# Optimization experiments

Measured on AMD Instinct MI355X. Metric: run time of the kernel, lower is better.

Reference implementation:

```python
import jax, jax.numpy as jnp
import numpy as np

D_MODEL = 512
N_HEADS = 8
D_K = D_MODEL // N_HEADS


def setup_inputs() -> dict:
    key = jax.random.key(0)
    kq, kk, kv = jax.random.split(key, 3)
    shape = (4, 2048, D_MODEL)
    return {
        "Q": jax.random.normal(kq, shape, dtype=jnp.float32),
        "K": jax.random.normal(kk, shape, dtype=jnp.float32),
        "V": jax.random.normal(kv, shape, dtype=jnp.float32),
    }


def reference(Q, K, V):
    B, S, _ = Q.shape
    # [B, S, H, Dk] -> [B, H, S, Dk]
    q = Q.reshape(B, S, N_HEADS, D_K).transpose(0, 2, 1, 3)
    k = K.reshape(B, S, N_HEADS, D_K).transpose(0, 2, 1, 3)
    v = V.reshape(B, S, N_HEADS, D_K).transpose(0, 2, 1, 3)
    scale = 1.0 / (D_K ** 0.5)
    # [B, H, S, S] scores (faithful to original: full matrix materialized)
    scores = jnp.einsum("bhqd,bhkd->bhqk", q, k) * scale
    attn = jax.nn.softmax(scores, axis=-1)
    out = jnp.einsum("bhqk,bhkd->bhqd", attn, v)
    # [B, H, S, Dk] -> [B, S, D_MODEL]
    return out.transpose(0, 2, 1, 3).reshape(B, S, D_MODEL)
```

## Files before the change

### kernel.cpp

```cpp
#include <hip/hip_runtime.h>
#include <hip/hip_bf16.h>

#define SEQ    2048
#define DMODEL 512
#define NH     8
#define QBLK   128
#define KVB    64

#if __has_builtin(__builtin_amdgcn_exp2f)
#define EXPFN(x) __builtin_amdgcn_exp2f(x)
#define QSCALE 0.18033688011112042f
#else
#define EXPFN(x) __expf(x)
#define QSCALE 0.125f
#endif
#define THR 8.0f

typedef __attribute__((ext_vector_type(8)))  short bf16x8;
typedef __attribute__((ext_vector_type(16))) float f32x16;
typedef __attribute__((ext_vector_type(2)))  int   i32x2;

#define MFMA32(A, B, C) __builtin_amdgcn_mfma_f32_32x32x16_bf16(A, B, C, 0, 0, 0)

__device__ __forceinline__ unsigned short f2bf(float f) {
  union { float f; unsigned u; } x; x.f = f;
  return (unsigned short)((x.u + 0x7FFFu + ((x.u >> 16) & 1u)) >> 16);
}

__device__ __forceinline__ int cvtpk(float lo, float hi) {
  int r;
  asm("v_cvt_pk_bf16_f32 %0, %1, %2" : "=v"(r) : "v"(lo), "v"(hi));
  return r;
}

__device__ __forceinline__ i32x2 plswap(int a, int b) {
#if __has_builtin(__builtin_amdgcn_permlane32_swap)
  return __builtin_amdgcn_permlane32_swap(a, b, false, false);
#else
  int a2 = __shfl_xor(a, 32), b2 = __shfl_xor(b, 32);
  int hi = (threadIdx.x >> 5) & 1;
  i32x2 r; r.x = hi ? b2 : a; r.y = hi ? b : a2; return r;
#endif
}

__device__ __forceinline__ void gload16(const void* g, void* l) {
  __builtin_amdgcn_global_load_lds(
      (const __attribute__((address_space(1))) void*)g,
      (__attribute__((address_space(3))) void*)l, 16, 0, 0);
}


__global__ void prep_kv(const float* __restrict__ K, const float* __restrict__ V,
                        unsigned short* __restrict__ kb, unsigned short* __restrict__ vb) {
  if (blockIdx.x < 2048) {
    int gid = blockIdx.x * 256 + threadIdx.x;
    int g  = gid & 7;
    int s  = (gid >> 3) & (SEQ - 1);
    int bh = gid >> 14;
    int b = bh >> 3, h = bh & 7;
    const float* src = K + ((size_t)(b * SEQ + s) * DMODEL) + h * 64 + (g << 3);
    float4 a = ((const float4*)src)[0];
    float4 c = ((const float4*)src)[1];
    bf16x8 w;
    w[0] = (short)f2bf(a.x); w[1] = (short)f2bf(a.y);
    w[2] = (short)f2bf(a.z); w[3] = (short)f2bf(a.w);
    w[4] = (short)f2bf(c.x); w[5] = (short)f2bf(c.y);
    w[6] = (short)f2bf(c.z); w[7] = (short)f2bf(c.w);
    int r = s & 63;
    int slot = ((((r >> 5) << 3) + g) ^ (r & 15));
    unsigned short* dst = kb + ((size_t)bh * SEQ + (s & ~63)) * 64
                             + ((r & 31) << 7) + (slot << 3);
    *(bf16x8*)dst = w;
  } else {
    int bt = blockIdx.x - 2048;
    int bh = bt >> 5, tile = bt & 31;
    int b = bh >> 3, h = bh & 7;
    int t  = threadIdx.x;
    int d  = t & 63;
    int kg = t >> 6;
    const float* src = V + ((size_t)(b * SEQ + tile * 64 + kg * 16) * DMODEL) + h * 64 + d;
    float v[16];
#pragma unroll
    for (int j = 0; j < 16; ++j) v[j] = src[(size_t)j * DMODEL];
    bf16x8 lo, hi;
#pragma unroll
    for (int j = 0; j < 8; ++j) { lo[j] = (short)f2bf(v[j]); hi[j] = (short)f2bf(v[8 + j]); }
    unsigned short* base = vb + ((size_t)bt << 12);
    int g0 = kg << 1, g1 = (kg << 1) | 1;
    int rb = (((d >> 5) << 3));
    int s0 = ((rb + g0) ^ (d & 15));
    int s1 = ((rb + g1) ^ (d & 15));
    unsigned short* row = base + ((d & 31) << 7);
    *(bf16x8*)(row + (s0 << 3)) = lo;
    *(bf16x8*)(row + (s1 << 3)) = hi;
  }
}

__global__ __launch_bounds__(256, 2)
void fa_fwd(const float* __restrict__ Q, const unsigned short* __restrict__ Kb,
            const unsigned short* __restrict__ Vb, float* __restrict__ O) {
  __shared__ unsigned short kt[2][KVB * 64];
  __shared__ unsigned short vt[2][64 * KVB];

  const int tid = threadIdx.x;
  const int wv  = tid >> 6;
  const int ln  = tid & 63;
  const int l31 = ln & 31;
  const int hi  = ln >> 5;

  const int orig = blockIdx.x;
  const int wgid = (orig & 7) * 64 + (orig >> 3);
  const int bh = wgid >> 4;
  const int qt = wgid & 15;
  const int b = bh >> 3, h = bh & 7;

  const float* Qh = Q + (size_t)b * SEQ * DMODEL + (size_t)h * 64;
  float*       Oh = O + (size_t)b * SEQ * DMODEL + (size_t)h * 64;
  const unsigned short* Kh = Kb + (size_t)bh * SEQ * 64;
  const unsigned short* Vh = Vb + (size_t)bh * SEQ * 64;

  const int q = qt * QBLK + wv * 32 + l31;

  bf16x8 qf[4];
  {
    const float* qp = Qh + (size_t)q * DMODEL + (hi << 3);
#pragma unroll
    for (int t = 0; t < 4; ++t) {
      float4 a = *(const float4*)(qp + 16 * t);
      float4 c = *(const float4*)(qp + 16 * t + 4);
      bf16x8 w;
      w[0] = (short)f2bf(a.x * QSCALE); w[1] = (short)f2bf(a.y * QSCALE);
      w[2] = (short)f2bf(a.z * QSCALE); w[3] = (short)f2bf(a.w * QSCALE);
      w[4] = (short)f2bf(c.x * QSCALE); w[5] = (short)f2bf(c.y * QSCALE);
      w[6] = (short)f2bf(c.z * QSCALE); w[7] = (short)f2bf(c.w * QSCALE);
      qf[t] = w;
    }
  }

  const int rowb = l31 << 7;
  int ca[4], cb[4];
#pragma unroll
  for (int t = 0; t < 4; ++t) {
    int g = 2 * t + hi;
    ca[t] = rowb + (((g)     ^ (l31 & 15)) << 3);
    cb[t] = rowb + (((8 + g) ^ (l31 & 15)) << 3);
  }

  f32x16 o0 = {}, o1 = {};
  float m = -__builtin_inff();
  float l = 0.f;

#define STAGE(T, B)                                                        \
  do {                                                                     \
    const char* gk = (const char*)(Kh + (size_t)(T) * KVB * 64);           \
    const char* gv = (const char*)(Vh + (size_t)(T) * KVB * 64);           \
    char* lk = (char*)&kt[(B)][0];                                         \
    char* lv = (char*)&vt[(B)][0];                                         \
    gload16(gk + (((wv)     * 64 + ln) << 4), lk + ((wv)     << 10));      \
    gload16(gk + (((wv + 4) * 64 + ln) << 4), lk + ((wv + 4) << 10));      \
    gload16(gv + (((wv)     * 64 + ln) << 4), lv + ((wv)     << 10));      \
    gload16(gv + (((wv + 4) * 64 + ln) << 4), lv + ((wv + 4) << 10));      \
  } while (0)

  auto tile_compute = [&](const unsigned short* ktb, const unsigned short* vtb) {
    f32x16 s0 = {}, s1 = {};
#pragma unroll
    for (int ks = 0; ks < 4; ++ks) {
      bf16x8 k0 = *(const bf16x8*)&ktb[ca[ks]];
      bf16x8 k1 = *(const bf16x8*)&ktb[cb[ks]];
      __builtin_amdgcn_s_setprio(1);
      s0 = MFMA32(k0, qf[ks], s0);
      s1 = MFMA32(k1, qf[ks], s1);
      __builtin_amdgcn_s_setprio(0);
    }

    float pm = fmaxf(s0[0], s0[1]);
#pragma unroll
    for (int j = 2; j < 16; ++j) pm = fmaxf(pm, s0[j]);
#pragma unroll
    for (int j = 0; j < 16; ++j) pm = fmaxf(pm, s1[j]);
    pm = fmaxf(pm, __shfl_xor(pm, 32));

    if (__any(pm > m + THR)) {
      float mn   = fmaxf(m, pm);
      float corr = EXPFN(m - mn);
      m = mn;
      l *= corr;
#pragma unroll
      for (int j = 0; j < 16; ++j) { o0[j] *= corr; o1[j] *= corr; }
    }

#pragma unroll
    for (int ks = 0; ks < 4; ++ks) {
      float e[8];
#pragma unroll
      for (int j = 0; j < 8; ++j) {
        float sv = (ks < 2) ? s0[(ks & 1) * 8 + j] : s1[(ks & 1) * 8 + j];
        e[j] = EXPFN(sv - m);
      }
      l += ((e[0] + e[1]) + (e[2] + e[3])) + ((e[4] + e[5]) + (e[6] + e[7]));
      i32x2 r0 = plswap(cvtpk(e[0], e[1]), cvtpk(e[4], e[5]));
      i32x2 r1 = plswap(cvtpk(e[2], e[3]), cvtpk(e[6], e[7]));
      union { int i[4]; bf16x8 v; } pa;
      pa.i[0] = r0.x; pa.i[1] = r1.x; pa.i[2] = r0.y; pa.i[3] = r1.y;

      bf16x8 v0 = *(const bf16x8*)&vtb[ca[ks]];
      bf16x8 v1 = *(const bf16x8*)&vtb[cb[ks]];
      __builtin_amdgcn_s_setprio(1);
      o0 = MFMA32(v0, pa.v, o0);
      o1 = MFMA32(v1, pa.v, o1);
      __builtin_amdgcn_s_setprio(0);
    }
  };

  STAGE(0, 0);
  __syncthreads();

  for (int t = 0; t < SEQ / KVB; t += 2) {
    STAGE(t + 1, 1);
    tile_compute(kt[0], vt[0]);
    __syncthreads();
    if (t + 2 < SEQ / KVB) STAGE(t + 2, 0);
    tile_compute(kt[1], vt[1]);
    __syncthreads();
  }

  l += __shfl_xor(l, 32);
  float rinv = 1.0f / l;
  float* op = Oh + (size_t)q * DMODEL;
#pragma unroll
  for (int r4 = 0; r4 < 4; ++r4) {
    float4 w0, w1;
    w0.x = o0[4 * r4 + 0] * rinv; w0.y = o0[4 * r4 + 1] * rinv;
    w0.z = o0[4 * r4 + 2] * rinv; w0.w = o0[4 * r4 + 3] * rinv;
    w1.x = o1[4 * r4 + 0] * rinv; w1.y = o1[4 * r4 + 1] * rinv;
    w1.z = o1[4 * r4 + 2] * rinv; w1.w = o1[4 * r4 + 3] * rinv;
    *(float4*)(op + 8 * r4 + 4 * hi)      = w0;
    *(float4*)(op + 32 + 8 * r4 + 4 * hi) = w1;
  }
}

extern "C" void kernel_launch(void* const* d_in, const int* in_sizes, int n_in,
                              void* d_out, int out_size, void* d_ws, size_t ws_size,
                              hipStream_t stream) {
  const float* Q = (const float*)d_in[0];
  const float* K = (const float*)d_in[1];
  const float* V = (const float*)d_in[2];
  float* O = (float*)d_out;
  unsigned short* kb = (unsigned short*)d_ws;
  unsigned short* vb = kb + (size_t)32 * SEQ * 64;
  prep_kv<<<3072, 256, 0, stream>>>(K, V, kb, vb);
  fa_fwd<<<512, 256, 0, stream>>>(Q, kb, vb, O);
}
```

Before: 63.12 us.

## Software-pipeline QK of next tile with softmax/PV of current tile

Splits the per-tile compute into a QK stage and a softmax+PV stage, and issues the QK MFMAs for tile t+1 before the softmax and PV of tile t so matrix work overlaps with exp/reduction work. LDS staging grows from double to quadruple buffering, with loads issued two tiles ahead. This doubles shared memory use and keeps two score accumulator sets live, which raises register pressure and could hurt occupancy at two blocks per CU.

```diff
diff --git a/kernel.cpp b/kernel.cpp
--- a/kernel.cpp
+++ b/kernel.cpp
@@ -6,6 +6,7 @@
 #define NH     8
 #define QBLK   128
 #define KVB    64
+#define NT     (SEQ / KVB)
 
 #if __has_builtin(__builtin_amdgcn_exp2f)
 #define EXPFN(x) __builtin_amdgcn_exp2f(x)
@@ -99,8 +100,8 @@
 __global__ __launch_bounds__(256, 2)
 void fa_fwd(const float* __restrict__ Q, const unsigned short* __restrict__ Kb,
             const unsigned short* __restrict__ Vb, float* __restrict__ O) {
-  __shared__ unsigned short kt[2][KVB * 64];
-  __shared__ unsigned short vt[2][64 * KVB];
+  __shared__ unsigned short kt[4][KVB * 64];
+  __shared__ unsigned short vt[4][64 * KVB];
 
   const int tid = threadIdx.x;
   const int wv  = tid >> 6;
@@ -147,6 +148,7 @@
   }
 
   f32x16 o0 = {}, o1 = {};
+  f32x16 sA0, sA1, sB0, sB1;
   float m = -__builtin_inff();
   float l = 0.f;
 
@@ -162,18 +164,21 @@
     gload16(gv + (((wv + 4) * 64 + ln) << 4), lv + ((wv + 4) << 10));      \
   } while (0)
 
-  auto tile_compute = [&](const unsigned short* ktb, const unsigned short* vtb) {
-    f32x16 s0 = {}, s1 = {};
+  auto qk = [&](const unsigned short* ktb, f32x16& t0, f32x16& t1) {
+    f32x16 u0 = {}, u1 = {};
 #pragma unroll
     for (int ks = 0; ks < 4; ++ks) {
       bf16x8 k0 = *(const bf16x8*)&ktb[ca[ks]];
       bf16x8 k1 = *(const bf16x8*)&ktb[cb[ks]];
       __builtin_amdgcn_s_setprio(1);
-      s0 = MFMA32(k0, qf[ks], s0);
-      s1 = MFMA32(k1, qf[ks], s1);
+      u0 = MFMA32(k0, qf[ks], u0);
+      u1 = MFMA32(k1, qf[ks], u1);
       __builtin_amdgcn_s_setprio(0);
     }
-
+    t0 = u0; t1 = u1;
+  };
+
+  auto smpv = [&](f32x16& s0, f32x16& s1, const unsigned short* vtb) {
     float pm = fmaxf(s0[0], s0[1]);
 #pragma unroll
     for (int j = 2; j < 16; ++j) pm = fmaxf(pm, s0[j]);
@@ -213,16 +218,24 @@
     }
   };
 
+#define ITER(T, BC, BN, BS, SC0, SC1, SN0, SN1)                            \
+  do {                                                                     \
+    if ((T) + 2 < NT) STAGE((T) + 2, BS);                                  \
+    if ((T) + 1 < NT) qk(kt[BN], SN0, SN1);                                \
+    smpv(SC0, SC1, vt[BC]);                                                \
+    __syncthreads();                                                       \
+  } while (0)
+
   STAGE(0, 0);
+  STAGE(1, 1);
   __syncthreads();
-
-  for (int t = 0; t < SEQ / KVB; t += 2) {
-    STAGE(t + 1, 1);
-    tile_compute(kt[0], vt[0]);
-    __syncthreads();
-    if (t + 2 < SEQ / KVB) STAGE(t + 2, 0);
-    tile_compute(kt[1], vt[1]);
-    __syncthreads();
+  qk(kt[0], sA0, sA1);
+
+  for (int t = 0; t < NT; t += 4) {
+    ITER(t + 0, 0, 1, 2, sA0, sA1, sB0, sB1);
+    ITER(t + 1, 1, 2, 3, sB0, sB1, sA0, sA1);
+    ITER(t + 2, 2, 3, 0, sA0, sA1, sB0, sB1);
+    ITER(t + 3, 3, 0, 1, sB0, sB1, sA0, sA1);
   }
 
   l += __shfl_xor(l, 32);
```

After: 63.30 us. About the same (+0.3%).

## Split KV sequence in two halves with fp16 partials and a combine kernel

Applied to the files above, without the earlier changes.

Adds a split-KV (flash-decoding style) path: each workgroup handles half of the key/value tiles for a query block, writing normalized fp16 partial outputs plus (max, sum) statistics, and a separate combine kernel merges the two halves into the fp32 output. This doubles the grid from 512 to 1024 workgroups with higher occupancy hints, so the GPU's CUs are better filled. The cost is an extra kernel launch, extra workspace traffic for the partials, and fp16 rounding of the partial outputs. The path only runs when the workspace is large enough; otherwise the original kernel is used.

```diff
diff --git a/kernel.cpp b/kernel.cpp
--- a/kernel.cpp
+++ b/kernel.cpp
@@ -1,11 +1,14 @@
 #include <hip/hip_runtime.h>
 #include <hip/hip_bf16.h>
+#include <hip/hip_fp16.h>
 
 #define SEQ    2048
 #define DMODEL 512
 #define NH     8
 #define QBLK   128
 #define KVB    64
+#define NT     (SEQ / KVB)
+#define NT_H   (NT / 2)
 
 #if __has_builtin(__builtin_amdgcn_exp2f)
 #define EXPFN(x) __builtin_amdgcn_exp2f(x)
@@ -16,9 +19,11 @@
 #endif
 #define THR 8.0f
 
-typedef __attribute__((ext_vector_type(8)))  short bf16x8;
-typedef __attribute__((ext_vector_type(16))) float f32x16;
-typedef __attribute__((ext_vector_type(2)))  int   i32x2;
+typedef __attribute__((ext_vector_type(8)))  short     bf16x8;
+typedef __attribute__((ext_vector_type(16))) float     f32x16;
+typedef __attribute__((ext_vector_type(2)))  int       i32x2;
+typedef __attribute__((ext_vector_type(4)))  _Float16  f16x4;
+typedef __attribute__((ext_vector_type(8)))  _Float16  f16x8;
 
 #define MFMA32(A, B, C) __builtin_amdgcn_mfma_f32_32x32x16_bf16(A, B, C, 0, 0, 0)
 
@@ -48,7 +53,6 @@
       (const __attribute__((address_space(1))) void*)g,
       (__attribute__((address_space(3))) void*)l, 16, 0, 0);
 }
-
 
 __global__ void prep_kv(const float* __restrict__ K, const float* __restrict__ V,
                         unsigned short* __restrict__ kb, unsigned short* __restrict__ vb) {
@@ -96,61 +100,7 @@
   }
 }
 
-__global__ __launch_bounds__(256, 2)
-void fa_fwd(const float* __restrict__ Q, const unsigned short* __restrict__ Kb,
-            const unsigned short* __restrict__ Vb, float* __restrict__ O) {
-  __shared__ unsigned short kt[2][KVB * 64];
-  __shared__ unsigned short vt[2][64 * KVB];
-
-  const int tid = threadIdx.x;
-  const int wv  = tid >> 6;
-  const int ln  = tid & 63;
-  const int l31 = ln & 31;
-  const int hi  = ln >> 5;
-
-  const int orig = blockIdx.x;
-  const int wgid = (orig & 7) * 64 + (orig >> 3);
-  const int bh = wgid >> 4;
-  const int qt = wgid & 15;
-  const int b = bh >> 3, h = bh & 7;
-
-  const float* Qh = Q + (size_t)b * SEQ * DMODEL + (size_t)h * 64;
-  float*       Oh = O + (size_t)b * SEQ * DMODEL + (size_t)h * 64;
-  const unsigned short* Kh = Kb + (size_t)bh * SEQ * 64;
-  const unsigned short* Vh = Vb + (size_t)bh * SEQ * 64;
-
-  const int q = qt * QBLK + wv * 32 + l31;
-
-  bf16x8 qf[4];
-  {
-    const float* qp = Qh + (size_t)q * DMODEL + (hi << 3);
-#pragma unroll
-    for (int t = 0; t < 4; ++t) {
-      float4 a = *(const float4*)(qp + 16 * t);
-      float4 c = *(const float4*)(qp + 16 * t + 4);
-      bf16x8 w;
-      w[0] = (short)f2bf(a.x * QSCALE); w[1] = (short)f2bf(a.y * QSCALE);
-      w[2] = (short)f2bf(a.z * QSCALE); w[3] = (short)f2bf(a.w * QSCALE);
-      w[4] = (short)f2bf(c.x * QSCALE); w[5] = (short)f2bf(c.y * QSCALE);
-      w[6] = (short)f2bf(c.z * QSCALE); w[7] = (short)f2bf(c.w * QSCALE);
-      qf[t] = w;
-    }
-  }
-
-  const int rowb = l31 << 7;
-  int ca[4], cb[4];
-#pragma unroll
-  for (int t = 0; t < 4; ++t) {
-    int g = 2 * t + hi;
-    ca[t] = rowb + (((g)     ^ (l31 & 15)) << 3);
-    cb[t] = rowb + (((8 + g) ^ (l31 & 15)) << 3);
-  }
-
-  f32x16 o0 = {}, o1 = {};
-  float m = -__builtin_inff();
-  float l = 0.f;
-
-#define STAGE(T, B)                                                        \
+#define STAGE_BODY(T, B)                                                   \
   do {                                                                     \
     const char* gk = (const char*)(Kh + (size_t)(T) * KVB * 64);           \
     const char* gv = (const char*)(Vh + (size_t)(T) * KVB * 64);           \
@@ -162,6 +112,61 @@
     gload16(gv + (((wv + 4) * 64 + ln) << 4), lv + ((wv + 4) << 10));      \
   } while (0)
 
+__global__ __launch_bounds__(256, 4)
+void fa_fwd_split(const float* __restrict__ Q, const unsigned short* __restrict__ Kb,
+                  const unsigned short* __restrict__ Vb,
+                  _Float16* __restrict__ opart, float2* __restrict__ ml) {
+  __shared__ unsigned short kt[2][KVB * 64];
+  __shared__ unsigned short vt[2][64 * KVB];
+
+  const int tid = threadIdx.x;
+  const int wv  = tid >> 6;
+  const int ln  = tid & 63;
+  const int l31 = ln & 31;
+  const int hi  = ln >> 5;
+
+  const int orig = blockIdx.x;
+  const int wgid = (orig & 7) * 128 + (orig >> 3);
+  const int bh   = wgid >> 5;
+  const int qt   = (wgid >> 1) & 15;
+  const int half = wgid & 1;
+  const int b = bh >> 3, h = bh & 7;
+
+  const float* Qh = Q + (size_t)b * SEQ * DMODEL + (size_t)h * 64;
+  const unsigned short* Kh = Kb + (size_t)bh * SEQ * 64 + (size_t)half * NT_H * KVB * 64;
+  const unsigned short* Vh = Vb + (size_t)bh * SEQ * 64 + (size_t)half * NT_H * KVB * 64;
+
+  const int qrow = qt * QBLK + wv * 32 + l31;
+
+  bf16x8 qf[4];
+  {
+    const float* qp = Qh + (size_t)qrow * DMODEL + (hi << 3);
+#pragma unroll
+    for (int t = 0; t < 4; ++t) {
+      float4 a = *(const float4*)(qp + 16 * t);
+      float4 c = *(const float4*)(qp + 16 * t + 4);
+      bf16x8 w;
+      w[0] = (short)f2bf(a.x * QSCALE); w[1] = (short)f2bf(a.y * QSCALE);
+      w[2] = (short)f2bf(a.z * QSCALE); w[3] = (short)f2bf(a.w * QSCALE);
+      w[4] = (short)f2bf(c.x * QSCALE); w[5] = (short)f2bf(c.y * QSCALE);
+      w[6] = (short)f2bf(c.z * QSCALE); w[7] = (short)f2bf(c.w * QSCALE);
+      qf[t] = w;
+    }
+  }
+
+  const int rowb = l31 << 7;
+  int ca[4], cb[4];
+#pragma unroll
+  for (int t = 0; t < 4; ++t) {
+    int g = 2 * t + hi;
+    ca[t] = rowb + (((g)     ^ (l31 & 15)) << 3);
+    cb[t] = rowb + (((8 + g) ^ (l31 & 15)) << 3);
+  }
+
+  f32x16 o0 = {}, o1 = {};
+  float m = -__builtin_inff();
+  float l = 0.f;
+
   auto tile_compute = [&](const unsigned short* ktb, const unsigned short* vtb) {
     f32x16 s0 = {}, s1 = {};
 #pragma unroll
@@ -213,14 +218,178 @@
     }
   };
 
-  STAGE(0, 0);
+  STAGE_BODY(0, 0);
   __syncthreads();
-
-  for (int t = 0; t < SEQ / KVB; t += 2) {
-    STAGE(t + 1, 1);
+  for (int t = 0; t < NT_H; t += 2) {
+    STAGE_BODY(t + 1, 1);
     tile_compute(kt[0], vt[0]);
     __syncthreads();
-    if (t + 2 < SEQ / KVB) STAGE(t + 2, 0);
+    if (t + 2 < NT_H) STAGE_BODY(t + 2, 0);
+    tile_compute(kt[1], vt[1]);
+    __syncthreads();
+  }
+
+  l += __shfl_xor(l, 32);
+  float rinv = 1.0f / l;
+  const size_t row = (size_t)bh * SEQ + qrow;
+  if (hi == 0) ml[(size_t)half * 32 * SEQ + row] = float2{m, l};
+  _Float16* op = opart + (size_t)half * 32 * SEQ * 64 + row * 64;
+#pragma unroll
+  for (int r4 = 0; r4 < 4; ++r4) {
+    f16x4 w0, w1;
+#pragma unroll
+    for (int j = 0; j < 4; ++j) {
+      w0[j] = (_Float16)(o0[4 * r4 + j] * rinv);
+      w1[j] = (_Float16)(o1[4 * r4 + j] * rinv);
+    }
+    *(f16x4*)(op + 8 * r4 + 4 * hi)      = w0;
+    *(f16x4*)(op + 32 + 8 * r4 + 4 * hi) = w1;
+  }
+}
+
+__global__ __launch_bounds__(256)
+void fa_combine(const _Float16* __restrict__ opart, const float2* __restrict__ ml,
+                float* __restrict__ O) {
+  int idx  = blockIdx.x * 256 + threadIdx.x;
+  int dg   = idx & 7;
+  int qrow = (idx >> 3) & (SEQ - 1);
+  int bh   = idx >> 14;
+  size_t row = (size_t)bh * SEQ + qrow;
+
+  float2 a = ml[row];
+  float2 c = ml[(size_t)32 * SEQ + row];
+  float M  = fmaxf(a.x, c.x);
+  float w1 = a.y * EXPFN(a.x - M);
+  float w2 = c.y * EXPFN(c.x - M);
+  float inv = 1.0f / (w1 + w2);
+  w1 *= inv; w2 *= inv;
+
+  f16x8 h1 = *(const f16x8*)(opart + row * 64 + dg * 8);
+  f16x8 h2 = *(const f16x8*)(opart + (size_t)32 * SEQ * 64 + row * 64 + dg * 8);
+
+  int b = bh >> 3, h = bh & 7;
+  float* out = O + ((size_t)(b * SEQ + qrow)) * DMODEL + h * 64 + dg * 8;
+  float4 v0, v1;
+  v0.x = w1 * (float)h1[0] + w2 * (float)h2[0];
+  v0.y = w1 * (float)h1[1] + w2 * (float)h2[1];
+  v0.z = w1 * (float)h1[2] + w2 * (float)h2[2];
+  v0.w = w1 * (float)h1[3] + w2 * (float)h2[3];
+  v1.x = w1 * (float)h1[4] + w2 * (float)h2[4];
+  v1.y = w1 * (float)h1[5] + w2 * (float)h2[5];
+  v1.z = w1 * (float)h1[6] + w2 * (float)h2[6];
+  v1.w = w1 * (float)h1[7] + w2 * (float)h2[7];
+  ((float4*)out)[0] = v0;
+  ((float4*)out)[1] = v1;
+}
+
+__global__ __launch_bounds__(256, 2)
+void fa_fwd(const float* __restrict__ Q, const unsigned short* __restrict__ Kb,
+            const unsigned short* __restrict__ Vb, float* __restrict__ O) {
+  __shared__ unsigned short kt[2][KVB * 64];
+  __shared__ unsigned short vt[2][64 * KVB];
+
+  const int tid = threadIdx.x;
+  const int wv  = tid >> 6;
+  const int ln  = tid & 63;
+  const int l31 = ln & 31;
+  const int hi  = ln >> 5;
+
+  const int orig = blockIdx.x;
+  const int wgid = (orig & 7) * 64 + (orig >> 3);
+  const int bh = wgid >> 4;
+  const int qt = wgid & 15;
+  const int b = bh >> 3, h = bh & 7;
+
+  const float* Qh = Q + (size_t)b * SEQ * DMODEL + (size_t)h * 64;
+  float*       Oh = O + (size_t)b * SEQ * DMODEL + (size_t)h * 64;
+  const unsigned short* Kh = Kb + (size_t)bh * SEQ * 64;
+  const unsigned short* Vh = Vb + (size_t)bh * SEQ * 64;
+
+  const int q = qt * QBLK + wv * 32 + l31;
+
+  bf16x8 qf[4];
+  {
+    const float* qp = Qh + (size_t)q * DMODEL + (hi << 3);
+#pragma unroll
+    for (int t = 0; t < 4; ++t) {
+      float4 a = *(const float4*)(qp + 16 * t);
+      float4 c = *(const float4*)(qp + 16 * t + 4);
+      bf16x8 w;
+      w[0] = (short)f2bf(a.x * QSCALE); w[1] = (short)f2bf(a.y * QSCALE);
+      w[2] = (short)f2bf(a.z * QSCALE); w[3] = (short)f2bf(a.w * QSCALE);
+      w[4] = (short)f2bf(c.x * QSCALE); w[5] = (short)f2bf(c.y * QSCALE);
+      w[6] = (short)f2bf(c.z * QSCALE); w[7] = (short)f2bf(c.w * QSCALE);
+      qf[t] = w;
+    }
+  }
+
+  const int rowb = l31 << 7;
+  int ca[4], cb[4];
+#pragma unroll
+  for (int t = 0; t < 4; ++t) {
+    int g = 2 * t + hi;
+    ca[t] = rowb + (((g)     ^ (l31 & 15)) << 3);
+    cb[t] = rowb + (((8 + g) ^ (l31 & 15)) << 3);
+  }
+
+  f32x16 o0 = {}, o1 = {};
+  float m = -__builtin_inff();
+  float l = 0.f;
+
+  auto tile_compute = [&](const unsigned short* ktb, const unsigned short* vtb) {
+    f32x16 s0 = {}, s1 = {};
+#pragma unroll
+    for (int ks = 0; ks < 4; ++ks) {
+      bf16x8 k0 = *(const bf16x8*)&ktb[ca[ks]];
+      bf16x8 k1 = *(const bf16x8*)&ktb[cb[ks]];
+      __builtin_amdgcn_s_setprio(1);
+      s0 = MFMA32(k0, qf[ks], s0);
+      s1 = MFMA32(k1, qf[ks], s1);
+      __builtin_amdgcn_s_setprio(0);
+    }
+    float pm = fmaxf(s0[0], s0[1]);
+#pragma unroll
+    for (int j = 2; j < 16; ++j) pm = fmaxf(pm, s0[j]);
+#pragma unroll
+    for (int j = 0; j < 16; ++j) pm = fmaxf(pm, s1[j]);
+    pm = fmaxf(pm, __shfl_xor(pm, 32));
+    if (__any(pm > m + THR)) {
+      float mn   = fmaxf(m, pm);
+      float corr = EXPFN(m - mn);
+      m = mn;
+      l *= corr;
+#pragma unroll
+      for (int j = 0; j < 16; ++j) { o0[j] *= corr; o1[j] *= corr; }
+    }
+#pragma unroll
+    for (int ks = 0; ks < 4; ++ks) {
+      float e[8];
+#pragma unroll
+      for (int j = 0; j < 8; ++j) {
+        float sv = (ks < 2) ? s0[(ks & 1) * 8 + j] : s1[(ks & 1) * 8 + j];
+        e[j] = EXPFN(sv - m);
+      }
+      l += ((e[0] + e[1]) + (e[2] + e[3])) + ((e[4] + e[5]) + (e[6] + e[7]));
+      i32x2 r0 = plswap(cvtpk(e[0], e[1]), cvtpk(e[4], e[5]));
+      i32x2 r1 = plswap(cvtpk(e[2], e[3]), cvtpk(e[6], e[7]));
+      union { int i[4]; bf16x8 v; } pa;
+      pa.i[0] = r0.x; pa.i[1] = r1.x; pa.i[2] = r0.y; pa.i[3] = r1.y;
+      bf16x8 v0 = *(const bf16x8*)&vtb[ca[ks]];
+      bf16x8 v1 = *(const bf16x8*)&vtb[cb[ks]];
+      __builtin_amdgcn_s_setprio(1);
+      o0 = MFMA32(v0, pa.v, o0);
+      o1 = MFMA32(v1, pa.v, o1);
+      __builtin_amdgcn_s_setprio(0);
+    }
+  };
+
+  STAGE_BODY(0, 0);
+  __syncthreads();
+  for (int t = 0; t < NT; t += 2) {
+    STAGE_BODY(t + 1, 1);
+    tile_compute(kt[0], vt[0]);
+    __syncthreads();
+    if (t + 2 < NT) STAGE_BODY(t + 2, 0);
     tile_compute(kt[1], vt[1]);
     __syncthreads();
   }
@@ -247,8 +416,21 @@
   const float* K = (const float*)d_in[1];
   const float* V = (const float*)d_in[2];
   float* O = (float*)d_out;
+
   unsigned short* kb = (unsigned short*)d_ws;
   unsigned short* vb = kb + (size_t)32 * SEQ * 64;
   prep_kv<<<3072, 256, 0, stream>>>(K, V, kb, vb);
-  fa_fwd<<<512, 256, 0, stream>>>(Q, kb, vb, O);
-}
+
+  const size_t base   = (size_t)2 * 32 * SEQ * 64 * sizeof(unsigned short);
+  const size_t needsp = base + (size_t)2 * 32 * SEQ * 64 * sizeof(_Float16)
+                              + (size_t)2 * 32 * SEQ * sizeof(float2);
+  if (ws_size >= needsp + (1u << 20)) {
+    _Float16* opart = (_Float16*)((char*)d_ws + base);
+    float2*   ml    = (float2*)((char*)d_ws + base +
+                       (size_t)2 * 32 * SEQ * 64 * sizeof(_Float16));
+    fa_fwd_split<<<1024, 256, 0, stream>>>(Q, kb, vb, opart, ml);
+    fa_combine<<<2048, 256, 0, stream>>>(opart, ml, O);
+  } else {
+    fa_fwd<<<512, 256, 0, stream>>>(Q, kb, vb, O);
+  }
+}
```

Result: slower. 70.60 us (+11.9%).

## Deepen K/V prefetch to four LDS buffers with vmcnt-based waits

Applied to the files above, without the earlier changes.

Expands the K/V shared-memory ring from two to four buffers and prefetches two tiles ahead. Per-tile __syncthreads are replaced with explicit s_waitcnt vmcnt counts plus s_barrier and sched_barriers, so in-flight loads are only waited on when needed. The goal is to hide global-to-LDS latency better. It doubles LDS use to 64KB per block, which may still allow two blocks per CU. Buffer reuse also relies on a single barrier per tile for correctness.

```diff
diff --git a/kernel.cpp b/kernel.cpp
--- a/kernel.cpp
+++ b/kernel.cpp
@@ -6,6 +6,7 @@
 #define NH     8
 #define QBLK   128
 #define KVB    64
+#define NT     (SEQ / KVB)
 
 #if __has_builtin(__builtin_amdgcn_exp2f)
 #define EXPFN(x) __builtin_amdgcn_exp2f(x)
@@ -16,11 +17,12 @@
 #endif
 #define THR 8.0f
 
-typedef __attribute__((ext_vector_type(8)))  short bf16x8;
-typedef __attribute__((ext_vector_type(16))) float f32x16;
-typedef __attribute__((ext_vector_type(2)))  int   i32x2;
+typedef __attribute__((ext_vector_type(8)))  short     bf16x8;
+typedef __attribute__((ext_vector_type(16))) float     f32x16;
+typedef __attribute__((ext_vector_type(2)))  int       i32x2;
 
 #define MFMA32(A, B, C) __builtin_amdgcn_mfma_f32_32x32x16_bf16(A, B, C, 0, 0, 0)
+#define VMCNT(n) asm volatile("s_waitcnt vmcnt(" #n ")" ::: "memory")
 
 __device__ __forceinline__ unsigned short f2bf(float f) {
   union { float f; unsigned u; } x; x.f = f;
@@ -48,7 +50,6 @@
       (const __attribute__((address_space(1))) void*)g,
       (__attribute__((address_space(3))) void*)l, 16, 0, 0);
 }
-
 
 __global__ void prep_kv(const float* __restrict__ K, const float* __restrict__ V,
                         unsigned short* __restrict__ kb, unsigned short* __restrict__ vb) {
@@ -99,8 +100,8 @@
 __global__ __launch_bounds__(256, 2)
 void fa_fwd(const float* __restrict__ Q, const unsigned short* __restrict__ Kb,
             const unsigned short* __restrict__ Vb, float* __restrict__ O) {
-  __shared__ unsigned short kt[2][KVB * 64];
-  __shared__ unsigned short vt[2][64 * KVB];
+  __shared__ unsigned short kt[4][KVB * 64];
+  __shared__ unsigned short vt[4][64 * KVB];
 
   const int tid = threadIdx.x;
   const int wv  = tid >> 6;
@@ -213,17 +214,38 @@
     }
   };
 
+#define ITER_FULL(T, BS, BC)                                               \
+  do {                                                                     \
+    STAGE((T) + 2, BS);                                                    \
+    __builtin_amdgcn_sched_barrier(0);                                     \
+    VMCNT(8);                                                              \
+    __builtin_amdgcn_s_barrier();                                          \
+    __builtin_amdgcn_sched_barrier(0);                                     \
+    tile_compute(kt[BC], vt[BC]);                                          \
+  } while (0)
+
+  __builtin_amdgcn_sched_barrier(0);
   STAGE(0, 0);
-  __syncthreads();
-
-  for (int t = 0; t < SEQ / KVB; t += 2) {
-    STAGE(t + 1, 1);
-    tile_compute(kt[0], vt[0]);
-    __syncthreads();
-    if (t + 2 < SEQ / KVB) STAGE(t + 2, 0);
-    tile_compute(kt[1], vt[1]);
-    __syncthreads();
-  }
+  STAGE(1, 1);
+
+  for (int t = 0; t < NT - 4; t += 4) {
+    ITER_FULL(t + 0, 2, 0);
+    ITER_FULL(t + 1, 3, 1);
+    ITER_FULL(t + 2, 0, 2);
+    ITER_FULL(t + 3, 1, 3);
+  }
+  ITER_FULL(NT - 4, 2, 0);
+  ITER_FULL(NT - 3, 3, 1);
+  __builtin_amdgcn_sched_barrier(0);
+  VMCNT(4);
+  __builtin_amdgcn_s_barrier();
+  __builtin_amdgcn_sched_barrier(0);
+  tile_compute(kt[2], vt[2]);
+  __builtin_amdgcn_sched_barrier(0);
+  VMCNT(0);
+  __builtin_amdgcn_s_barrier();
+  __builtin_amdgcn_sched_barrier(0);
+  tile_compute(kt[3], vt[3]);
 
   l += __shfl_xor(l, 32);
   float rinv = 1.0f / l;
```

Result: no change. 63.06 us (-0.1%).
